# Kernel tuning notes

Hardware: AMD Instinct MI355X
Metric: run time of the kernel (lower is better)

The kernel has to match this reference:

```python
import jax, jax.numpy as jnp
import numpy as np
from jax import lax

H = 32      # n_heads
D = 128     # head_dim
HID = 4096  # hidden_dim
CQ, CK, CH = 4, 9, 2
G = H // CH  # conv groups == groupnorm groups == 16


def setup_inputs() -> dict:
    key = jax.random.key(0)
    ks = jax.random.split(key, 8)
    q_seqlen = np.array([512, 384, 384, 256], dtype=np.int64)
    kv_seqlen = np.array([512, 384, 384, 256], dtype=np.int64)
    Sq = int(q_seqlen.sum())
    Sk = int(kv_seqlen.sum())
    x = jax.random.normal(ks[0], (Sq, HID), dtype=jnp.float32) * 0.02
    context = jax.random.normal(ks[1], (Sk, HID), dtype=jnp.float32) * 0.02
    wq = jax.random.normal(ks[2], (HID, H * D), dtype=jnp.float32) * 0.02
    wkv = jax.random.normal(ks[3], (HID, 2 * H * D), dtype=jnp.float32) * 0.02
    wo = jax.random.normal(ks[4], (H * D, HID), dtype=jnp.float32) * 0.02
    # grouped conv kernel [out=H, in_per_group=CH, CQ, CK]; dirac-like identity + noise
    conv_w = jax.random.normal(ks[5], (H, CH, CQ, CK), dtype=jnp.float32) * 0.05
    conv_w = conv_w.at[jnp.arange(H), jnp.arange(H) % CH, CQ // 2, CK // 2].add(1.0)
    gn_w = jnp.ones((H,), dtype=jnp.float32)
    gn_b = jnp.zeros((H,), dtype=jnp.float32)
    return {"x": x, "context": context, "wq": wq, "wkv": wkv, "wo": wo,
            "conv_w": conv_w, "gn_w": gn_w, "gn_b": gn_b,
            "q_seqlen": q_seqlen, "kv_seqlen": kv_seqlen}


def _block_diag_mask(q_seqlen, kv_seqlen, dtype):
    # block-diagonal ones mask for packed ragged sequences (static lengths)
    q_len = np.asarray(q_seqlen)
    k_len = np.asarray(kv_seqlen)
    seg_q = np.repeat(np.arange(len(q_len)), q_len)
    seg_k = np.repeat(np.arange(len(k_len)), k_len)
    return jnp.asarray(seg_q[:, None] == seg_k[None, :], dtype=dtype)


def reference(x, context, wq, wkv, wo, conv_w, gn_w, gn_b, q_seqlen, kv_seqlen):
    S = x.shape[0]
    mask = _block_diag_mask(q_seqlen, kv_seqlen, x.dtype)  # [Sq, Sk]
    scale = 1.0 / np.sqrt(D).astype(np.float32)
    q = (x @ wq).reshape(S, H, D).transpose(1, 0, 2) * scale        # [H, Sq, D]
    kv = context @ wkv
    k = kv[:, : H * D].reshape(-1, H, D).transpose(1, 0, 2)         # [H, Sk, D]
    v = kv[:, H * D :].reshape(-1, H, D).transpose(1, 0, 2)         # [H, Sk, D]
    attn = jnp.einsum('hqd,hkd->hqk', q, k) * mask[None]            # [H, Sq, Sk]
    # grouped Conv2d over (query, key) positions, channels = heads
    a = lax.conv_general_dilated(
        attn[None], conv_w, window_strides=(1, 1),
        padding=((CQ // 2, CQ // 2), (CK // 2, CK // 2)),
        dimension_numbers=('NCHW', 'OIHW', 'NCHW'),
        feature_group_count=G)[0]                                   # [H, Sq+1, Sk]
    a = a[:, :-1, :]  # c_q even -> drop extra row (c_k odd -> no col drop)
    a = jax.nn.softmax(a + mask[None], axis=-1)                     # note: +1 bias inside blocks, not -inf
    out = jnp.einsum('hqk,hkd->hqd', a, v)                          # [H, Sq, D]
    # GroupNorm(num_groups=G, channels=H) over [1, H, Sq, D]
    og = out.reshape(G, CH, S, D)
    mu = og.mean(axis=(1, 2, 3), keepdims=True)
    var = og.var(axis=(1, 2, 3), keepdims=True)
    og = (og - mu) * lax.rsqrt(var + 1e-5)
    out = og.reshape(H, S, D) * gn_w[:, None, None] + gn_b[:, None, None]
    out = out.transpose(1, 0, 2).reshape(S, H * D)
    return out @ wo
```

## Files before the change

### kernel.cpp

```cpp
#include <hip/hip_runtime.h>
#include <stdint.h>


#define H_   32
#define D_   128
#define HID_ 4096
#define WMAX2 944
#define LPAD 8

typedef unsigned short bfr;
typedef __attribute__((ext_vector_type(4))) float f32x4;
typedef __attribute__((ext_vector_type(4))) int   i32x4;
typedef __attribute__((ext_vector_type(8))) unsigned short u16x8;
typedef __attribute__((ext_vector_type(4))) unsigned short u16x4;

__device__ __forceinline__ bfr f2bf(float f) {
  uint32_t u = __float_as_uint(f);
  u += 0x7fffu + ((u >> 16) & 1u);
  return (bfr)(u >> 16);
}
__device__ __forceinline__ float bf2f(bfr u) {
  return __uint_as_float(((uint32_t)u) << 16);
}
__device__ __forceinline__ void mfma_bf16(f32x4& d, i32x4 a, i32x4 b) {
  asm volatile("v_mfma_f32_16x16x32_bf16 %0, %1, %2, %0" : "+v"(d) : "v"(a), "v"(b));
}
__device__ __forceinline__ void gload_lds16(const void* g, void* l) {
  __builtin_amdgcn_global_load_lds((__attribute__((address_space(1))) void*)g,
                                   (__attribute__((address_space(3))) void*)l,
                                   16, 0, 0);
}

__global__ __launch_bounds__(256) void seg_setup(
    const void* __restrict__ qsl, const void* __restrict__ ksl,
    int* __restrict__ segq, int* __restrict__ segk,
    int* __restrict__ bq, int* __restrict__ bk,
    float* __restrict__ stats, int S, int Sk, int nseg)
{
  __shared__ int sbq[16], sbk[16];
  const int tid = threadIdx.x;
  if (tid == 0) {
    {
      const int* q32 = (const int*)qsl;
      long long s32 = 0; bool ok32 = true;
      for (int i = 0; i < nseg; ++i) { int v = q32[i]; if (v < 1 || v > S) ok32 = false; s32 += v; }
      const bool use32 = ok32 && (s32 == S);
      const long long* q64 = (const long long*)qsl;
      sbq[0] = 0;
      for (int i = 0; i < nseg; ++i) sbq[i + 1] = sbq[i] + (use32 ? q32[i] : (int)q64[i]);
    }
    {
      const int* k32 = (const int*)ksl;
      long long s32 = 0; bool ok32 = true;
      for (int i = 0; i < nseg; ++i) { int v = k32[i]; if (v < 1 || v > Sk) ok32 = false; s32 += v; }
      const bool use32 = ok32 && (s32 == Sk);
      const long long* k64 = (const long long*)ksl;
      sbk[0] = 0;
      for (int i = 0; i < nseg; ++i) sbk[i + 1] = sbk[i] + (use32 ? k32[i] : (int)k64[i]);
    }
    for (int i = 0; i <= nseg; ++i) { bq[i] = sbq[i]; bk[i] = sbk[i]; }
  }
  if (tid < 32) stats[tid] = 0.f;
  __syncthreads();
  for (int i = tid; i < S; i += 256) {
    int s = 0;
    while (s < nseg - 1 && i >= sbq[s + 1]) ++s;
    segq[i] = s;
  }
  for (int i = tid; i < Sk; i += 256) {
    int s = 0;
    while (s < nseg - 1 && i >= sbk[s + 1]) ++s;
    segk[i] = s;
  }
}

__global__ __launch_bounds__(256) void cvt_bf16(
    const float* __restrict__ in, bfr* __restrict__ out, long long n)
{
  long long i = ((long long)blockIdx.x * 256 + threadIdx.x) * 8;
  if (i >= n) return;
  f32x4 a = *(const f32x4*)(in + i);
  f32x4 b = *(const f32x4*)(in + i + 4);
  u16x8 o;
  #pragma unroll
  for (int j = 0; j < 4; ++j) { o[j] = f2bf(a[j]); o[4 + j] = f2bf(b[j]); }
  *(u16x8*)(out + i) = o;
}

__global__ __launch_bounds__(256) void transpose_cvt(
    const float* __restrict__ in, bfr* __restrict__ out, int R, int ld)
{
  __shared__ float tile[64][65];
  const int t = threadIdx.x;
  const int rb = blockIdx.y * 64, cb = blockIdx.x * 64;
  const int row = t >> 2, c4 = (t & 3) * 16;
  const float* gp = in + (long long)(rb + row) * ld + cb + c4;
  #pragma unroll
  for (int j = 0; j < 4; ++j) {
    f32x4 v = *(const f32x4*)(gp + j * 4);
    #pragma unroll
    for (int q = 0; q < 4; ++q) tile[row][c4 + j * 4 + q] = v[q];
  }
  __syncthreads();
  const int cc = row, r4 = c4;
  u16x8 a, b;
  #pragma unroll
  for (int j = 0; j < 8; ++j) a[j] = f2bf(tile[r4 + j][cc]);
  #pragma unroll
  for (int j = 0; j < 8; ++j) b[j] = f2bf(tile[r4 + 8 + j][cc]);
  bfr* op = out + (long long)(cb + cc) * R + rb + r4;
  *(u16x8*)op = a;
  *(u16x8*)(op + 8) = b;
}

__global__ __launch_bounds__(256) void transpose_b16(
    const bfr* __restrict__ in, bfr* __restrict__ out, int R, int C)
{
  __shared__ bfr t[64][72];
  const int z = blockIdx.z;
  const bfr* ip = in + (long long)z * R * C;
  bfr* op = out + (long long)z * R * C;
  const int rb = blockIdx.y * 64, cb = blockIdx.x * 64;
  const int tr = threadIdx.x >> 3;
  const int tc = (threadIdx.x & 7) * 8;
  #pragma unroll
  for (int half = 0; half < 2; ++half) {
    const int r = tr + half * 32;
    u16x8 v = *(const u16x8*)(ip + (long long)(rb + r) * C + cb + tc);
    *(u16x8*)&t[r][tc] = v;
  }
  __syncthreads();
  #pragma unroll
  for (int half = 0; half < 2; ++half) {
    const int cc = tr + half * 32;
    u16x8 vv;
    #pragma unroll
    for (int j = 0; j < 8; ++j) vv[j] = t[tc + j][cc];
    *(u16x8*)(op + (long long)(cb + cc) * R + rb + tc) = vv;
  }
}

__global__ __launch_bounds__(256) void colsum_v(
    const bfr* __restrict__ vt, float* __restrict__ cs, int Sk)
{
  const int lane = threadIdx.x & 63, wave = threadIdx.x >> 6;
  const int row = blockIdx.x * 4 + wave;
  const bfr* src = vt + (long long)row * Sk;
  float s = 0.f;
  for (int i = lane * 8; i + 8 <= Sk; i += 512) {
    u16x8 v = *(const u16x8*)(src + i);
    #pragma unroll
    for (int j = 0; j < 8; ++j) s += bf2f(v[j]);
  }
  #pragma unroll
  for (int m = 1; m < 64; m <<= 1) s += __shfl_xor(s, m);
  if (lane == 0) cs[row] = s;
}

struct GemmAux {
  const int* segq; const int* segk; const int* bk;
  bfr* qb; bfr* kb; bfr* vrow;
  float* outb; float* stats;
  const float* fvArr; const float* colsum;
  float scale;
  int S, Sk, nOff;
};

enum { MODE_PLAIN = 0, MODE_Q = 1, MODE_KV = 2, MODE_QK = 3, MODE_PV = 4 };

template <int MODE>
__global__ __launch_bounds__(256) void gemm_bt(
    const bfr* __restrict__ A, const bfr* __restrict__ Bt, void* __restrict__ Cout,
    int N, int K, int lda, int ldb,
    long long aZ, long long bZ, long long cZ, GemmAux aux)
{
  __shared__ bfr As[128 * 32];
  __shared__ bfr Bs[128 * 32];
  __shared__ float redS[8], redSS[8];
  const int tid = threadIdx.x;
  const int lane = tid & 63;
  const int wave = tid >> 6;
  const int z = blockIdx.z;

  int bx = blockIdx.x, by = blockIdx.y;
  {
    const int gx = gridDim.x, gy = gridDim.y;
    if (((gx & 3) == 0) && ((gy & 1) == 0)) {
      const int lid = by * gx + bx;
      const int xcd = lid & 7, inner = lid >> 3;
      const int cm = gy >> 1, cn = gx >> 2;
      by = (xcd >> 2) * cm + inner / cn;
      bx = (xcd & 3) * cn + inner % cn;
    }
  }
  const int m0 = by * 128;
  const int n0 = bx * 128;
  const bfr* Ap = A + (long long)z * aZ;
  const bfr* Bp = Bt + (long long)z * bZ;

  if constexpr (MODE == MODE_QK) {
    const int t127 = min(m0 + 127, aux.S - 1);
    const int loT = max(aux.bk[aux.segq[max(m0 - 2, 0)]] - 4, 0);
    const int hiT = min(aux.bk[aux.segq[min(t127 + 1, aux.S - 1)] + 1] + 4, aux.Sk);
    if (n0 > hiT + 16 || n0 + 127 < loT - 16) return;
    const int sm0 = aux.segq[m0], sm1 = aux.segq[t127];
    const int sn0 = aux.segk[n0], sn1 = aux.segk[min(n0 + 127, aux.Sk - 1)];
    if (sm1 < sn0 || sn1 < sm0) {
      bfr* C = (bfr*)Cout + (long long)z * cZ + (long long)m0 * aux.Sk + n0;
      const i32x4 zz = {0, 0, 0, 0};
      #pragma unroll
      for (int c = 0; c < 8; ++c) {
        int id = c * 256 + tid;
        int r = id >> 4, col = (id & 15) * 8;
        *(i32x4*)(C + (long long)r * aux.Sk + col) = zz;
      }
      return;
    }
  }

  int kLo = 0, kHiV = K;
  if constexpr (MODE == MODE_PV) {
    const int t127 = min(m0 + 127, aux.S - 1);
    kLo = (max(aux.bk[aux.segq[max(m0 - 2, 0)]] - 4, 0)) & ~31;
    int th = min(aux.bk[aux.segq[min(t127 + 1, aux.S - 1)] + 1] + 4, aux.Sk);
    kHiV = min((th + 31) & ~31, aux.Sk);
  }

  const int wr = (wave >> 1) * 64;
  const int wc = (wave & 1) * 64;
  f32x4 acc[4][4];
  #pragma unroll
  for (int i = 0; i < 4; ++i)
    #pragma unroll
    for (int j = 0; j < 4; ++j) acc[i][j] = (f32x4){0.f, 0.f, 0.f, 0.f};

  const int kSteps = (kHiV - kLo) >> 5;
  for (int ks = 0; ks < kSteps; ++ks) {
    const int k0 = kLo + (ks << 5);
    #pragma unroll
    for (int c = 0; c < 4; ++c) {
      const int chunk = (wave << 2) + c;
      const int ci = chunk & 7;
      const int row = ci * 16 + (lane >> 2);
      const int col = (lane & 3) * 8;
      if (chunk < 8) gload_lds16(Ap + (long long)(m0 + row) * lda + k0 + col, As + ci * 512);
      else           gload_lds16(Bp + (long long)(n0 + row) * ldb + k0 + col, Bs + ci * 512);
    }
    __syncthreads();
    i32x4 af[4], bfv[4];
    #pragma unroll
    for (int i = 0; i < 4; ++i)
      af[i] = *(const i32x4*)&As[(wr + i * 16 + (lane & 15)) * 32 + (lane >> 4) * 8];
    #pragma unroll
    for (int i = 0; i < 4; ++i)
      bfv[i] = *(const i32x4*)&Bs[(wc + i * 16 + (lane & 15)) * 32 + (lane >> 4) * 8];
    #pragma unroll
    for (int i = 0; i < 4; ++i)
      #pragma unroll
      for (int j = 0; j < 4; ++j)
        mfma_bf16(acc[i][j], af[i], bfv[j]);
    __syncthreads();
  }

  bool qkUni = false;
  int sgm[16], sgn[4];
  float fvm[16], csn[4];
  if constexpr (MODE == MODE_QK) {
    const int sA = aux.segq[m0], sB = aux.segq[min(m0 + 127, aux.S - 1)];
    const int sC = aux.segk[n0], sD = aux.segk[min(n0 + 127, aux.Sk - 1)];
    qkUni = (sA == sB) && (sC == sD);
    if (!qkUni) {
      #pragma unroll
      for (int i = 0; i < 4; ++i)
        #pragma unroll
        for (int r = 0; r < 4; ++r)
          sgm[i * 4 + r] = aux.segq[m0 + wr + i * 16 + (lane >> 4) * 4 + r];
      #pragma unroll
      for (int j = 0; j < 4; ++j) sgn[j] = aux.segk[n0 + wc + j * 16 + (lane & 15)];
    }
  }
  if constexpr (MODE == MODE_PV) {
    #pragma unroll
    for (int i = 0; i < 4; ++i)
      #pragma unroll
      for (int r = 0; r < 4; ++r)
        fvm[i * 4 + r] = aux.fvArr[(long long)z * aux.S + m0 + wr + i * 16 + (lane >> 4) * 4 + r];
    #pragma unroll
    for (int j = 0; j < 4; ++j)
      csn[j] = aux.colsum[(long long)z * D_ + n0 + wc + j * 16 + (lane & 15)];
  }

  float sv = 0.f, sq2 = 0.f;
  #pragma unroll
  for (int i = 0; i < 4; ++i) {
    #pragma unroll
    for (int j = 0; j < 4; ++j) {
      #pragma unroll
      for (int r = 0; r < 4; ++r) {
        const int m = m0 + wr + i * 16 + (lane >> 4) * 4 + r;
        const int n = n0 + wc + j * 16 + (lane & 15);
        const float v = acc[i][j][r];
        if constexpr (MODE == MODE_PLAIN) {
          ((float*)Cout)[(long long)m * N + n] = v;
        } else if constexpr (MODE == MODE_Q) {
          const int hh = n >> 7, d = n & 127;
          aux.qb[((long long)hh * aux.S + m) * D_ + d] = f2bf(v * aux.scale);
        } else if constexpr (MODE == MODE_KV) {
          const int ng = n + aux.nOff;
          if (ng < H_ * D_) {
            const int hh = ng >> 7, d = ng & 127;
            aux.kb[((long long)hh * aux.Sk + m) * D_ + d] = f2bf(v);
          } else {
            const int nv = ng - H_ * D_;
            const int hh = nv >> 7, d = nv & 127;
            aux.vrow[((long long)hh * aux.Sk + m) * D_ + d] = f2bf(v);
          }
        } else if constexpr (MODE == MODE_QK) {
          const float vv = (qkUni || sgm[i * 4 + r] == sgn[j]) ? v : 0.f;
          ((bfr*)Cout)[(long long)z * cZ + (long long)m * aux.Sk + n] = f2bf(vv);
        } else if constexpr (MODE == MODE_PV) {
          const float vv = v + fvm[i * 4 + r] * csn[j];
          aux.outb[((long long)z * aux.S + m) * D_ + n] = vv;
          sv += vv; sq2 += vv * vv;
        }
      }
    }
  }

  if constexpr (MODE == MODE_PV) {
    #pragma unroll
    for (int msk = 1; msk < 64; msk <<= 1) {
      sv  += __shfl_xor(sv, msk);
      sq2 += __shfl_xor(sq2, msk);
    }
    if (lane == 0) { redS[wave] = sv; redSS[wave] = sq2; }
    __syncthreads();
    if (tid == 0) {
      const float a = redS[0] + redS[1] + redS[2] + redS[3];
      const float b = redSS[0] + redSS[1] + redSS[2] + redSS[3];
      atomicAdd(&aux.stats[(z >> 1) * 2 + 0], a);
      atomicAdd(&aux.stats[(z >> 1) * 2 + 1], b);
    }
  }
}

__global__ __launch_bounds__(256) void conv_softmax4(
    const bfr* __restrict__ attn, const float* __restrict__ conv_w,
    bfr* __restrict__ p, float* __restrict__ fvArr,
    const int* __restrict__ segq, const int* __restrict__ segk,
    const int* __restrict__ bk, int S, int Sk, int h0)
{
  __shared__ float wsh[144];
  __shared__ bfr sIn[7][WMAX2];
  const int tid = threadIdx.x, lane = tid & 63, w = tid >> 6;
  const int q0 = blockIdx.x * 4;
  const int c0 = blockIdx.y * 2;
  const int h  = h0 + c0;
  if (tid < 144) wsh[tid] = conv_w[h * 72 + tid];

  const int qlast = q0 + 3;
  const int lo0 = (max(bk[segq[max(q0 - 2, 0)]] - 4, 0)) & ~7;
  const int hiL = min(bk[segq[min(qlast + 1, S - 1)] + 1] + 4, Sk);
  const int g0 = max(lo0 - 8, 0) & ~7;
  const int g1 = min(hiL + 4, Sk);
  const int W8 = (g1 - g0 + 7) >> 3;

  const int qa = q0 + w;
  const int loA = (max(bk[segq[max(qa - 2, 0)]] - 4, 0)) & ~7;
  const int hiA = min(bk[segq[min(qa + 1, S - 1)] + 1] + 4, Sk);
  const int sqA = segq[qa];
  const int width = hiA - loA;

  float lg[2][4][4];
  #pragma unroll
  for (int e = 0; e < 2; ++e)
    #pragma unroll
    for (int pp = 0; pp < 4; ++pp)
      #pragma unroll
      for (int o = 0; o < 4; ++o) lg[e][pp][o] = 0.f;

  if (tid < 7) {
    const u16x8 zz8 = {0,0,0,0,0,0,0,0};
    *(u16x8*)&sIn[tid][0] = zz8;
    *(u16x8*)&sIn[tid][LPAD + W8 * 8] = zz8;
  }

  for (int pass = 0; pass < 2; ++pass) {
    if (pass) __syncthreads();
    const bfr* src0 = attn + (long long)(c0 + pass) * S * Sk;
    for (int it = tid; it < 7 * 116; it += 256) {
      const int ri = it / 116;
      const int j  = it - ri * 116;
      if (j < W8) {
        const int r = q0 - 2 + ri;
        u16x8 v = {0,0,0,0,0,0,0,0};
        if (r >= 0 && r < S) v = *(const u16x8*)(src0 + (long long)r * Sk + g0 + j * 8);
        *(u16x8*)&sIn[ri][LPAD + j * 8] = v;
      }
    }
    __syncthreads();

    #pragma unroll
    for (int pp = 0; pp < 4; ++pp) {
      const int kk = loA + pp * 256 + lane * 4;
      if (kk < hiA) {
        const int ib = LPAD + kk - 4 - g0;
        #pragma unroll
        for (int rr = 0; rr < 4; ++rr) {
          const bfr* sp = &sIn[w + rr][ib];
          u16x4 u0 = *(const u16x4*)(sp);
          u16x4 u1 = *(const u16x4*)(sp + 4);
          u16x4 u2 = *(const u16x4*)(sp + 8);
          float xx[12];
          #pragma unroll
          for (int j2 = 0; j2 < 4; ++j2) {
            xx[j2]     = bf2f(u0[j2]);
            xx[4 + j2] = bf2f(u1[j2]);
            xx[8 + j2] = bf2f(u2[j2]);
          }
          const float* wv0 = &wsh[(pass * 4 + rr) * 9];
          const float* wv1 = wv0 + 72;
          #pragma unroll
          for (int dk = 0; dk < 9; ++dk) {
            #pragma unroll
            for (int o = 0; o < 4; ++o) {
              lg[0][pp][o] += xx[o + dk] * wv0[dk];
              lg[1][pp][o] += xx[o + dk] * wv1[dk];
            }
          }
        }
      }
    }
  }

  float lmax0 = -1e30f, lmax1 = -1e30f;
  #pragma unroll
  for (int pp = 0; pp < 4; ++pp) {
    const int kk = loA + pp * 256 + lane * 4;
    i32x4 sk4 = {0, 0, 0, 0};
    if (kk < Sk) sk4 = *(const i32x4*)&segk[kk];
    #pragma unroll
    for (int o = 0; o < 4; ++o) {
      const int k = kk + o;
      float v0 = -1e30f, v1 = -1e30f;
      if (k < hiA) {
        const float mb = (sk4[o] == sqA) ? 1.f : 0.f;
        v0 = lg[0][pp][o] + mb; lmax0 = fmaxf(lmax0, v0);
        v1 = lg[1][pp][o] + mb; lmax1 = fmaxf(lmax1, v1);
      }
      lg[0][pp][o] = v0; lg[1][pp][o] = v1;
    }
  }
  #pragma unroll
  for (int m = 1; m < 64; m <<= 1) {
    lmax0 = fmaxf(lmax0, __shfl_xor(lmax0, m));
    lmax1 = fmaxf(lmax1, __shfl_xor(lmax1, m));
  }
  const float M0 = fmaxf(lmax0, 0.f), M1 = fmaxf(lmax1, 0.f);
  float ls0 = 0.f, ls1 = 0.f;
  #pragma unroll
  for (int pp = 0; pp < 4; ++pp)
    #pragma unroll
    for (int o = 0; o < 4; ++o) {
      const float e0 = __expf(lg[0][pp][o] - M0);
      const float e1 = __expf(lg[1][pp][o] - M1);
      lg[0][pp][o] = e0; ls0 += e0;
      lg[1][pp][o] = e1; ls1 += e1;
    }
  #pragma unroll
  for (int m = 1; m < 64; m <<= 1) {
    ls0 += __shfl_xor(ls0, m);
    ls1 += __shfl_xor(ls1, m);
  }
  const float eo0 = __expf(-M0), eo1 = __expf(-M1);
  const float iv0 = 1.f / (ls0 + (float)(Sk - width) * eo0);
  const float iv1 = 1.f / (ls1 + (float)(Sk - width) * eo1);
  const float fv0 = eo0 * iv0, fv1 = eo1 * iv1;

  const int t0 = (q0 >> 7) << 7;
  const int t127 = min(t0 + 127, S - 1);
  const int tLo = (max(bk[segq[max(t0 - 2, 0)]] - 4, 0)) & ~31;
  int tHi = min(bk[segq[min(t127 + 1, S - 1)] + 1] + 4, Sk);
  tHi = min((tHi + 31) & ~31, Sk);

  bfr* row0 = p + ((long long)(c0 + 0) * S + qa) * Sk;
  bfr* row1 = p + ((long long)(c0 + 1) * S + qa) * Sk;
  #pragma unroll
  for (int pp = 0; pp < 4; ++pp) {
    const int kk = loA + pp * 256 + lane * 4;
    if (kk + 3 < hiA) {
      u16x4 s0, s1;
      #pragma unroll
      for (int o = 0; o < 4; ++o) {
        s0[o] = f2bf(lg[0][pp][o] * iv0 - fv0);
        s1[o] = f2bf(lg[1][pp][o] * iv1 - fv1);
      }
      *(u16x4*)(row0 + kk) = s0;
      *(u16x4*)(row1 + kk) = s1;
    } else if (kk < hiA) {
      for (int o = 0; o < 4; ++o)
        if (kk + o < hiA) {
          row0[kk + o] = f2bf(lg[0][pp][o] * iv0 - fv0);
          row1[kk + o] = f2bf(lg[1][pp][o] * iv1 - fv1);
        }
    }
  }
  const u16x4 z4 = {0, 0, 0, 0};
  for (int k = tLo + lane * 4; k < loA; k += 256) {
    *(u16x4*)(row0 + k) = z4;
    *(u16x4*)(row1 + k) = z4;
  }
  for (int k = hiA + lane; k < tHi; k += 64) { row0[k] = 0; row1[k] = 0; }
  if (lane == 0) {
    fvArr[(long long)(h + 0) * S + qa] = fv0;
    fvArr[(long long)(h + 1) * S + qa] = fv1;
  }
}

__global__ void gn_finalize(const float* __restrict__ stats, float* __restrict__ mr, float invcnt)
{
  const int g = threadIdx.x;
  if (g < 16) {
    const float s = stats[2 * g], ss = stats[2 * g + 1];
    const float mu = s * invcnt;
    const float var = ss * invcnt - mu * mu;
    mr[2 * g] = mu;
    mr[2 * g + 1] = rsqrtf(var + 1e-5f);
  }
}

__global__ __launch_bounds__(256) void gn_apply(
    const float* __restrict__ outb, const float* __restrict__ mr,
    const float* __restrict__ gnw, const float* __restrict__ gnb,
    bfr* __restrict__ y, int S)
{
  const int h = blockIdx.y;
  const long long inner = ((long long)blockIdx.x * 256 + threadIdx.x) * 8;
  if (inner >= (long long)S * D_) return;
  const int s = (int)(inner >> 7), d = (int)(inner & 127);
  const int g = h >> 1;
  const float mu = mr[2 * g], rs = mr[2 * g + 1];
  const float wgt = gnw[h] * rs;
  const float b = gnb[h] - mu * wgt;
  const float* src = outb + (long long)h * S * D_ + inner;
  const f32x4 a = *(const f32x4*)(src);
  const f32x4 c = *(const f32x4*)(src + 4);
  u16x8 o;
  #pragma unroll
  for (int j = 0; j < 4; ++j) { o[j] = f2bf(a[j] * wgt + b); o[4 + j] = f2bf(c[j] * wgt + b); }
  *(u16x8*)(y + (long long)s * HID_ + h * D_ + d) = o;
}

extern "C" void kernel_launch(void* const* d_in, const int* in_sizes, int n_in,
                              void* d_out, int out_size, void* d_ws, size_t ws_size,
                              hipStream_t stream)
{
  const float* x      = (const float*)d_in[0];
  const float* ctx    = (const float*)d_in[1];
  const float* wq     = (const float*)d_in[2];
  const float* wkv    = (const float*)d_in[3];
  const float* wo     = (const float*)d_in[4];
  const float* conv_w = (const float*)d_in[5];
  const float* gnw    = (const float*)d_in[6];
  const float* gnb    = (const float*)d_in[7];
  const void*  qsl    = d_in[8];
  const void*  ksl    = d_in[9];
  const int S    = in_sizes[0] / HID_;
  const int Sk   = in_sizes[1] / HID_;
  const int nseg = in_sizes[8];

  auto al = [](size_t v) { return (v + 255) & ~(size_t)255; };
  char* base = (char*)d_ws;
  size_t off = 0;
  auto take = [&](size_t bytes) -> char* { char* r = base + off; off += al(bytes); return r; };

  int*   segq  = (int*)take((size_t)S * 4);
  int*   segk  = (int*)take((size_t)Sk * 4);
  int*   bq    = (int*)take(64);
  int*   bk    = (int*)take(64);
  float* stats = (float*)take(128);
  float* mr    = (float*)take(128);
  float* fvArr = (float*)take((size_t)H_ * S * 4);
  float* csV   = (float*)take((size_t)H_ * D_ * 4);
  bfr*   qb    = (bfr*)take((size_t)H_ * S * D_ * 2);
  bfr*   kbuf  = (bfr*)take((size_t)H_ * Sk * D_ * 2);
  bfr*   vrow  = (bfr*)take((size_t)H_ * Sk * D_ * 2);
  bfr*   vt    = (bfr*)take((size_t)H_ * Sk * D_ * 2);
  float* outb  = (float*)take((size_t)H_ * S * D_ * 4);
  const size_t poolBase = off;
  char*  pool  = base + poolBase;

  const int Smax = (S > Sk) ? S : Sk;
  const size_t A1 = al((size_t)Smax * HID_ * 2);
  const size_t WT = al((size_t)HID_ * HID_ * 2);

  const size_t CAmin = al((size_t)4 * S * Sk * 2);
  const size_t fusedNeed = (A1 + 2 * WT > 2 * CAmin) ? (A1 + 2 * WT) : (2 * CAmin);
  const bool fused = (poolBase + fusedNeed <= ws_size);
  const size_t wNeed = A1 + (fused ? 2 : 1) * WT;

  int nc = 4;
  {
    const int cands[3] = {32, 16, 8};
    for (int ci = 0; ci < 3; ++ci) {
      const size_t CA = al((size_t)cands[ci] * S * Sk * 2);
      const size_t need = (wNeed > 2 * CA) ? wNeed : (2 * CA);
      if (poolBase + need <= ws_size) { nc = cands[ci]; break; }
    }
  }
  const size_t CA = al((size_t)nc * S * Sk * 2);
  bfr* xcb    = (bfr*)pool;
  bfr* wT     = (bfr*)(pool + A1);
  bfr* attn_c = (bfr*)pool;
  bfr* pbuf_c = (bfr*)(pool + CA);

  seg_setup<<<1, 256, 0, stream>>>(qsl, ksl, segq, segk, bq, bk, stats, S, Sk, nseg);

  GemmAux aux{};
  aux.segq = segq; aux.segk = segk; aux.bk = bk;
  aux.qb = qb; aux.kb = kbuf; aux.vrow = vrow;
  aux.outb = outb; aux.stats = stats;
  aux.fvArr = fvArr; aux.colsum = csV;
  aux.scale = 0.08838834764831845f;
  aux.S = S; aux.Sk = Sk; aux.nOff = 0;

  const long long nx = (long long)S * HID_;
  cvt_bf16<<<(int)((nx / 8 + 255) / 256), 256, 0, stream>>>(x, xcb, nx);
  transpose_cvt<<<dim3(HID_ / 64, HID_ / 64), 256, 0, stream>>>(wq, wT, HID_, HID_);
  gemm_bt<MODE_Q><<<dim3(HID_ / 128, S / 128, 1), 256, 0, stream>>>(
      xcb, wT, nullptr, HID_, HID_, HID_, HID_, 0, 0, 0, aux);

  const long long nctx = (long long)Sk * HID_;
  cvt_bf16<<<(int)((nctx / 8 + 255) / 256), 256, 0, stream>>>(ctx, xcb, nctx);
  if (fused) {
    transpose_cvt<<<dim3(2 * HID_ / 64, HID_ / 64), 256, 0, stream>>>(wkv, wT, HID_, 2 * HID_);
    gemm_bt<MODE_KV><<<dim3(2 * HID_ / 128, Sk / 128, 1), 256, 0, stream>>>(
        xcb, wT, nullptr, 2 * HID_, HID_, HID_, HID_, 0, 0, 0, aux);
  } else {
    transpose_cvt<<<dim3(HID_ / 64, HID_ / 64), 256, 0, stream>>>(wkv, wT, HID_, 2 * HID_);
    gemm_bt<MODE_KV><<<dim3(HID_ / 128, Sk / 128, 1), 256, 0, stream>>>(
        xcb, wT, nullptr, HID_, HID_, HID_, HID_, 0, 0, 0, aux);
    transpose_cvt<<<dim3(HID_ / 64, HID_ / 64), 256, 0, stream>>>(wkv + HID_, wT, HID_, 2 * HID_);
    GemmAux auxV = aux; auxV.nOff = H_ * D_;
    gemm_bt<MODE_KV><<<dim3(HID_ / 128, Sk / 128, 1), 256, 0, stream>>>(
        xcb, wT, nullptr, HID_, HID_, HID_, HID_, 0, 0, 0, auxV);
  }

  transpose_b16<<<dim3(D_ / 64, Sk / 64, H_), 256, 0, stream>>>(vrow, vt, Sk, D_);
  colsum_v<<<H_ * D_ / 4, 256, 0, stream>>>(vt, csV, Sk);

  for (int h0 = 0; h0 < H_; h0 += nc) {
    gemm_bt<MODE_QK><<<dim3(Sk / 128, S / 128, nc), 256, 0, stream>>>(
        qb + (size_t)h0 * S * D_, kbuf + (size_t)h0 * Sk * D_, attn_c,
        Sk, D_, D_, D_,
        (long long)S * D_, (long long)Sk * D_, (long long)S * Sk, aux);
    conv_softmax4<<<dim3(S / 4, nc / 2), 256, 0, stream>>>(
        attn_c, conv_w, pbuf_c, fvArr, segq, segk, bk, S, Sk, h0);
    GemmAux auxP = aux;
    auxP.outb = outb + (size_t)h0 * S * D_;
    auxP.stats = stats + h0;
    auxP.fvArr = fvArr + (size_t)h0 * S;
    auxP.colsum = csV + (size_t)h0 * D_;
    gemm_bt<MODE_PV><<<dim3(1, S / 128, nc), 256, 0, stream>>>(
        pbuf_c, vt + (size_t)h0 * D_ * Sk, nullptr,
        D_, Sk, Sk, Sk,
        (long long)S * Sk, (long long)D_ * Sk, 0, auxP);
  }

  gn_finalize<<<1, 32, 0, stream>>>(stats, mr, 1.0f / (2.0f * S * D_));
  gn_apply<<<dim3((S * D_) / 2048, H_), 256, 0, stream>>>(outb, mr, gnw, gnb, xcb, S);
  transpose_cvt<<<dim3(HID_ / 64, HID_ / 64), 256, 0, stream>>>(wo, wT, HID_, HID_);
  gemm_bt<MODE_PLAIN><<<dim3(HID_ / 128, S / 128, 1), 256, 0, stream>>>(
      xcb, wT, d_out, HID_, HID_, HID_, HID_, 0, 0, 0, aux);
}
```

Baseline: 593.3 us.

## Split-K the Q and output projection GEMMs and swizzle LDS tiles

Adds a split-K template parameter to the GEMM. The Q and output projections now run as two K-halves written to an fp32 partial buffer, and a reduction kernel sums the halves and applies the scale and head layout. The aim is more workgroups on the CU-rich device, since these GEMMs produce only 32x12 tiles. The change also XOR-swizzles the LDS load and read columns to reduce bank conflicts. In exchange it adds extra fp32 partial writes and reads plus two more kernel launches, and needs more workspace.

```diff
diff --git a/kernel.cpp b/kernel.cpp
--- a/kernel.cpp
+++ b/kernel.cpp
@@ -168,7 +168,7 @@
 
 enum { MODE_PLAIN = 0, MODE_Q = 1, MODE_KV = 2, MODE_QK = 3, MODE_PV = 4 };
 
-template <int MODE>
+template <int MODE, int KS = 1>
 __global__ __launch_bounds__(256) void gemm_bt(
     const bfr* __restrict__ A, const bfr* __restrict__ Bt, void* __restrict__ Cout,
     int N, int K, int lda, int ldb,
@@ -219,6 +219,11 @@
   }
 
   int kLo = 0, kHiV = K;
+  if constexpr (KS > 1) {
+    const int kspan = K / KS;
+    kLo = z * kspan;
+    kHiV = kLo + kspan;
+  }
   if constexpr (MODE == MODE_PV) {
     const int t127 = min(m0 + 127, aux.S - 1);
     kLo = (max(aux.bk[aux.segq[max(m0 - 2, 0)]] - 4, 0)) & ~31;
@@ -234,6 +239,10 @@
     #pragma unroll
     for (int j = 0; j < 4; ++j) acc[i][j] = (f32x4){0.f, 0.f, 0.f, 0.f};
 
+  const int srow = lane >> 2;
+  const int scol = (((lane & 3) ^ ((lane >> 2) & 3)) << 3);
+  const int rcol = (((lane >> 4) ^ (lane & 3)) << 3);
+
   const int kSteps = (kHiV - kLo) >> 5;
   for (int ks = 0; ks < kSteps; ++ks) {
     const int k0 = kLo + (ks << 5);
@@ -241,19 +250,18 @@
     for (int c = 0; c < 4; ++c) {
       const int chunk = (wave << 2) + c;
       const int ci = chunk & 7;
-      const int row = ci * 16 + (lane >> 2);
-      const int col = (lane & 3) * 8;
-      if (chunk < 8) gload_lds16(Ap + (long long)(m0 + row) * lda + k0 + col, As + ci * 512);
-      else           gload_lds16(Bp + (long long)(n0 + row) * ldb + k0 + col, Bs + ci * 512);
+      const int row = ci * 16 + srow;
+      if (chunk < 8) gload_lds16(Ap + (long long)(m0 + row) * lda + k0 + scol, As + ci * 512);
+      else           gload_lds16(Bp + (long long)(n0 + row) * ldb + k0 + scol, Bs + ci * 512);
     }
     __syncthreads();
     i32x4 af[4], bfv[4];
     #pragma unroll
     for (int i = 0; i < 4; ++i)
-      af[i] = *(const i32x4*)&As[(wr + i * 16 + (lane & 15)) * 32 + (lane >> 4) * 8];
+      af[i] = *(const i32x4*)&As[(wr + i * 16 + (lane & 15)) * 32 + rcol];
     #pragma unroll
     for (int i = 0; i < 4; ++i)
-      bfv[i] = *(const i32x4*)&Bs[(wc + i * 16 + (lane & 15)) * 32 + (lane >> 4) * 8];
+      bfv[i] = *(const i32x4*)&Bs[(wc + i * 16 + (lane & 15)) * 32 + rcol];
     #pragma unroll
     for (int i = 0; i < 4; ++i)
       #pragma unroll
@@ -300,7 +308,9 @@
         const int m = m0 + wr + i * 16 + (lane >> 4) * 4 + r;
         const int n = n0 + wc + j * 16 + (lane & 15);
         const float v = acc[i][j][r];
-        if constexpr (MODE == MODE_PLAIN) {
+        if constexpr (KS > 1) {
+          aux.outb[((long long)z * aux.S + m) * N + n] = v;
+        } else if constexpr (MODE == MODE_PLAIN) {
           ((float*)Cout)[(long long)m * N + n] = v;
         } else if constexpr (MODE == MODE_Q) {
           const int hh = n >> 7, d = n & 127;
@@ -327,7 +337,7 @@
     }
   }
 
-  if constexpr (MODE == MODE_PV) {
+  if constexpr (MODE == MODE_PV && KS == 1) {
     #pragma unroll
     for (int msk = 1; msk < 64; msk <<= 1) {
       sv  += __shfl_xor(sv, msk);
@@ -344,6 +354,44 @@
   }
 }
 
+__global__ __launch_bounds__(256) void reduce_split_q(
+    const float* __restrict__ part, bfr* __restrict__ qb, float scale, int S)
+{
+  const long long MN = (long long)S * HID_;
+  const long long i = ((long long)blockIdx.x * 256 + threadIdx.x) * 8;
+  if (i >= MN) return;
+  const f32x4 a0 = *(const f32x4*)(part + i);
+  const f32x4 a1 = *(const f32x4*)(part + i + 4);
+  const f32x4 b0 = *(const f32x4*)(part + MN + i);
+  const f32x4 b1 = *(const f32x4*)(part + MN + i + 4);
+  const int m = (int)(i >> 12);
+  const int n = (int)(i & 4095);
+  const int hh = n >> 7, d = n & 127;
+  u16x8 o;
+  #pragma unroll
+  for (int j = 0; j < 4; ++j) {
+    o[j]     = f2bf((a0[j] + b0[j]) * scale);
+    o[4 + j] = f2bf((a1[j] + b1[j]) * scale);
+  }
+  *(u16x8*)(qb + ((long long)hh * S + m) * D_ + d) = o;
+}
+
+__global__ __launch_bounds__(256) void reduce_split_f32(
+    const float* __restrict__ part, float* __restrict__ out, long long MN)
+{
+  const long long i = ((long long)blockIdx.x * 256 + threadIdx.x) * 8;
+  if (i >= MN) return;
+  const f32x4 a0 = *(const f32x4*)(part + i);
+  const f32x4 a1 = *(const f32x4*)(part + i + 4);
+  const f32x4 b0 = *(const f32x4*)(part + MN + i);
+  const f32x4 b1 = *(const f32x4*)(part + MN + i + 4);
+  f32x4 o0, o1;
+  #pragma unroll
+  for (int j = 0; j < 4; ++j) { o0[j] = a0[j] + b0[j]; o1[j] = a1[j] + b1[j]; }
+  *(f32x4*)(out + i) = o0;
+  *(f32x4*)(out + i + 4) = o1;
+}
+
 __global__ __launch_bounds__(256) void conv_softmax4(
     const bfr* __restrict__ attn, const float* __restrict__ conv_w,
     bfr* __restrict__ p, float* __restrict__ fvArr,
@@ -358,9 +406,8 @@
   const int h  = h0 + c0;
   if (tid < 144) wsh[tid] = conv_w[h * 72 + tid];
 
-  const int qlast = q0 + 3;
   const int lo0 = (max(bk[segq[max(q0 - 2, 0)]] - 4, 0)) & ~7;
-  const int hiL = min(bk[segq[min(qlast + 1, S - 1)] + 1] + 4, Sk);
+  const int hiL = min(bk[segq[min(q0 + 4, S - 1)] + 1] + 4, Sk);
   const int g0 = max(lo0 - 8, 0) & ~7;
   const int g1 = min(hiL + 4, Sk);
   const int W8 = (g1 - g0 + 7) >> 3;
@@ -593,11 +640,13 @@
   const int Smax = (S > Sk) ? S : Sk;
   const size_t A1 = al((size_t)Smax * HID_ * 2);
   const size_t WT = al((size_t)HID_ * HID_ * 2);
+  const size_t PART = al((size_t)2 * S * HID_ * 4);
 
   const size_t CAmin = al((size_t)4 * S * Sk * 2);
   const size_t fusedNeed = (A1 + 2 * WT > 2 * CAmin) ? (A1 + 2 * WT) : (2 * CAmin);
   const bool fused = (poolBase + fusedNeed <= ws_size);
-  const size_t wNeed = A1 + (fused ? 2 : 1) * WT;
+  const bool splitOK = (poolBase + A1 + 2 * WT + PART <= ws_size);
+  const size_t wNeed = A1 + (fused ? 2 : 1) * WT + (splitOK ? PART : 0);
 
   int nc = 4;
   {
@@ -609,10 +658,11 @@
     }
   }
   const size_t CA = al((size_t)nc * S * Sk * 2);
-  bfr* xcb    = (bfr*)pool;
-  bfr* wT     = (bfr*)(pool + A1);
-  bfr* attn_c = (bfr*)pool;
-  bfr* pbuf_c = (bfr*)(pool + CA);
+  bfr*   xcb    = (bfr*)pool;
+  bfr*   wT     = (bfr*)(pool + A1);
+  float* partB  = (float*)(pool + A1 + 2 * WT);
+  bfr*   attn_c = (bfr*)pool;
+  bfr*   pbuf_c = (bfr*)(pool + CA);
 
   seg_setup<<<1, 256, 0, stream>>>(qsl, ksl, segq, segk, bq, bk, stats, S, Sk, nseg);
 
@@ -624,11 +674,21 @@
   aux.scale = 0.08838834764831845f;
   aux.S = S; aux.Sk = Sk; aux.nOff = 0;
 
+  const long long MN = (long long)S * HID_;
+  const int nRed = (int)((MN / 8 + 255) / 256);
+
   const long long nx = (long long)S * HID_;
   cvt_bf16<<<(int)((nx / 8 + 255) / 256), 256, 0, stream>>>(x, xcb, nx);
   transpose_cvt<<<dim3(HID_ / 64, HID_ / 64), 256, 0, stream>>>(wq, wT, HID_, HID_);
-  gemm_bt<MODE_Q><<<dim3(HID_ / 128, S / 128, 1), 256, 0, stream>>>(
-      xcb, wT, nullptr, HID_, HID_, HID_, HID_, 0, 0, 0, aux);
+  if (splitOK) {
+    GemmAux auxQ = aux; auxQ.outb = partB;
+    gemm_bt<MODE_Q, 2><<<dim3(HID_ / 128, S / 128, 2), 256, 0, stream>>>(
+        xcb, wT, nullptr, HID_, HID_, HID_, HID_, 0, 0, 0, auxQ);
+    reduce_split_q<<<nRed, 256, 0, stream>>>(partB, qb, aux.scale, S);
+  } else {
+    gemm_bt<MODE_Q><<<dim3(HID_ / 128, S / 128, 1), 256, 0, stream>>>(
+        xcb, wT, nullptr, HID_, HID_, HID_, HID_, 0, 0, 0, aux);
+  }
 
   const long long nctx = (long long)Sk * HID_;
   cvt_bf16<<<(int)((nctx / 8 + 255) / 256), 256, 0, stream>>>(ctx, xcb, nctx);
@@ -670,6 +730,13 @@
   gn_finalize<<<1, 32, 0, stream>>>(stats, mr, 1.0f / (2.0f * S * D_));
   gn_apply<<<dim3((S * D_) / 2048, H_), 256, 0, stream>>>(outb, mr, gnw, gnb, xcb, S);
   transpose_cvt<<<dim3(HID_ / 64, HID_ / 64), 256, 0, stream>>>(wo, wT, HID_, HID_);
-  gemm_bt<MODE_PLAIN><<<dim3(HID_ / 128, S / 128, 1), 256, 0, stream>>>(
-      xcb, wT, d_out, HID_, HID_, HID_, HID_, 0, 0, 0, aux);
-}
+  if (splitOK) {
+    GemmAux auxO = aux; auxO.outb = partB;
+    gemm_bt<MODE_PLAIN, 2><<<dim3(HID_ / 128, S / 128, 2), 256, 0, stream>>>(
+        xcb, wT, nullptr, HID_, HID_, HID_, HID_, 0, 0, 0, auxO);
+    reduce_split_f32<<<nRed, 256, 0, stream>>>(partB, (float*)d_out, MN);
+  } else {
+    gemm_bt<MODE_PLAIN><<<dim3(HID_ / 128, S / 128, 1), 256, 0, stream>>>(
+        xcb, wT, d_out, HID_, HID_, HID_, HID_, 0, 0, 0, aux);
+  }
+}
```

Result: faster. 544.0 us (-8.3%).
